# Optimization experiments

Measured on AMD Instinct MI355X. Metric: run time of the kernel, lower is better.

The kernel has to match this reference:

```python
import jax, jax.numpy as jnp
import numpy as np

ALPHA = 0.2      # GAT leaky_relu slope (args.alpha)
MLP_SLOPE = 0.01 # F.leaky_relu default in the MLP path
NEG = -9e15

def _l2_normalize(x, axis=1, eps=1e-12):
    n = jnp.sqrt(jnp.sum(x * x, axis=axis, keepdims=True))
    return x / jnp.maximum(n, eps)

def setup_inputs() -> dict:
    key = jax.random.key(0)
    ks = jax.random.split(key, 14)
    N, Din, Dh, H, Dg, M1, M2, E = 8192, 512, 256, 2, 512, 512, 256, 100000
    x = jax.random.normal(ks[0], (N, Din), dtype=jnp.float32)
    adj = jax.random.randint(ks[1], (N, N), 0, 2, dtype=jnp.int32)
    train_sample = jax.random.randint(ks[2], (E, 2), 0, N, dtype=jnp.int32)
    llm_emb = jax.random.normal(ks[3], (N, Dg), dtype=jnp.float32)
    # GAT head params (stacked over heads)
    Wg = jax.random.normal(ks[4], (H, Din, Dh), dtype=jnp.float32) * 0.05
    a1 = jax.random.normal(ks[5], (H, Dh), dtype=jnp.float32) * 0.05
    a2 = jax.random.normal(ks[6], (H, Dh), dtype=jnp.float32) * 0.05
    bias_g = jnp.zeros((H, Dh), dtype=jnp.float32)
    # MLP params
    W1 = jax.random.normal(ks[7], (Dh + Dg, M1), dtype=jnp.float32) * 0.03
    b1 = jnp.zeros((M1,), dtype=jnp.float32)
    W2 = jax.random.normal(ks[8], (M1, M2), dtype=jnp.float32) * 0.04
    b2 = jnp.zeros((M2,), dtype=jnp.float32)
    return {"x": x, "adj": adj, "train_sample": train_sample, "llm_emb": llm_emb,
            "Wg": Wg, "a1": a1, "a2": a2, "bias_g": bias_g,
            "W1": W1, "b1": b1, "W2": W2, "b2": b2}

def reference(x, adj, train_sample, llm_emb, Wg, a1, a2, bias_g, W1, b1, W2, b2):
    mask = adj > 0  # [N, N]

    def head(W, av1, av2, b):
        h = x @ W                                   # [N, Dh]
        s1 = h @ av1                                # [N]
        s2 = h @ av2                                # [N]
        e = jax.nn.leaky_relu(s1[:, None] + s2[None, :], ALPHA)  # [N, N]
        att = jax.nn.softmax(jnp.where(mask, e, NEG), axis=1)
        out = att @ h                               # [N, Dh]
        out = jax.nn.leaky_relu(out, ALPHA)
        out = _l2_normalize(out, axis=1)
        return out + b

    # encode: single GNN layer -> mean over heads (dropout inactive in eval)
    out_heads = jax.vmap(head)(Wg, a1, a2, bias_g)  # [H, N, Dh]
    embed_gnn = jnp.mean(out_heads, axis=0)         # [N, Dh]
    embed = jnp.concatenate([llm_emb, embed_gnn], axis=1)  # [N, Dg+Dh]

    def mlp(z):
        z = jax.nn.leaky_relu(z @ W1 + b1, MLP_SLOPE)
        z = jax.nn.leaky_relu(z @ W2 + b2, MLP_SLOPE)
        return z

    tf_embed = mlp(embed)
    target_embed = mlp(embed)
    train_tf = tf_embed[train_sample[:, 0]]
    train_tg = target_embed[train_sample[:, 1]]
    pred = jnp.sum(train_tf * train_tg, axis=1, keepdims=True)  # dot decode, [E,1]
    return pred
```

## Files before the change

kernel.cpp:

```cpp
#include <hip/hip_runtime.h>
#include <hip/hip_bf16.h>
#include <cstdint>
#include <cstddef>

#define ALPHA 0.2f
#define MLP_SLOPE 0.01f

typedef short bf16x8 __attribute__((ext_vector_type(8)));
typedef float f32x4 __attribute__((ext_vector_type(4)));
typedef unsigned short ushort_t;

#define ASM_BARRIER() __asm__ __volatile__("s_waitcnt lgkmcnt(0)\n\ts_barrier" ::: "memory")

__device__ __forceinline__ float lrelu(float x, float s) { return x > 0.f ? x : x * s; }
__device__ __forceinline__ ushort_t f2bf(float x) {
  __hip_bfloat16 h = __float2bfloat16(x);
  return *reinterpret_cast<ushort_t*>(&h);
}
__device__ __forceinline__ float bf2f(ushort_t u) {
  union { unsigned int i; float f; } v; v.i = ((unsigned int)u) << 16; return v.f;
}

__global__ __launch_bounds__(256) void tobf(
    const float* __restrict__ in, ushort_t* __restrict__ outp)
{
  int idx = blockIdx.x * 256 + threadIdx.x;
  float4 v = ((const float4*)in)[idx];
  ushort4 h;
  h.x = f2bf(v.x); h.y = f2bf(v.y); h.z = f2bf(v.z); h.w = f2bf(v.w);
  ((ushort4*)outp)[idx] = h;
}

__global__ __launch_bounds__(256) void zero_f(float* __restrict__ p)
{
  int idx = blockIdx.x * 256 + threadIdx.x;
  ((float4*)p)[idx] = make_float4(0.f, 0.f, 0.f, 0.f);
}

__global__ __launch_bounds__(256) void pack_wt(
    const float* __restrict__ W, ushort_t* __restrict__ hi,
    ushort_t* __restrict__ lo, int K, int N)
{
  int gid = blockIdx.x * 256 + threadIdx.x;
  int lane = gid & 63;
  int kbc = K >> 5;
  int kblk = (gid >> 6) % kbc;
  int nblk = (gid >> 6) / kbc;
  size_t b = (size_t)blockIdx.y * K * N;
  int col = nblk * 16 + (lane & 15);
  int krow = kblk * 32 + (lane >> 4) * 8;
  ushort_t h[8] __attribute__((aligned(16)));
  ushort_t l[8] __attribute__((aligned(16)));
#pragma unroll
  for (int e = 0; e < 8; ++e) {
    float v = W[b + (size_t)(krow + e) * N + col];
    h[e] = f2bf(v);
    l[e] = f2bf(v - bf2f(h[e]));
  }
  *(uint4*)&hi[b + (size_t)gid * 8] = *(uint4*)h;
  if (lo) *(uint4*)&lo[b + (size_t)gid * 8] = *(uint4*)l;
}

__global__ __launch_bounds__(256, 2) void gemm_h(
    const ushort_t* __restrict__ xb, const ushort_t* __restrict__ Wgp,
    const float* __restrict__ a1, const float* __restrict__ a2,
    ushort_t* __restrict__ Bpack, float* __restrict__ s1,
    float* __restrict__ s2)
{
  __shared__ ushort_t Ab[2][128][40];
  const int t = threadIdx.x;
  const int head = blockIdx.z;
  const int m0 = blockIdx.y * 128;
  const int n0 = blockIdx.x * 64;
  const int wave = t >> 6;
  const int wm = (wave & 1) * 64, wn = (wave >> 1) * 32;
  const int l16 = t & 15, quad = (t >> 4) & 3, l63 = t & 63;
  const int sr = t >> 1, sp = (t & 1) * 16;
  const ushort_t* arow_g = xb + (size_t)(m0 + sr) * 512 + sp;
  const ushort_t* bp = Wgp + (size_t)head * 256 * 512;
  const int nb0 = (n0 + wn) >> 4;

  f32x4 acc[4][2];
#pragma unroll
  for (int i = 0; i < 4; ++i)
#pragma unroll
    for (int j = 0; j < 2; ++j) acc[i][j] = (f32x4){0.f, 0.f, 0.f, 0.f};

  uint4 r0, r1;
  r0 = *(const uint4*)(arow_g);
  r1 = *(const uint4*)(arow_g + 8);
  *(uint4*)&Ab[0][sr][sp] = r0;
  *(uint4*)&Ab[0][sr][sp + 8] = r1;
  __syncthreads();

  for (int kb = 0; kb < 16; ++kb) {
    const int cur = kb & 1, nxt = cur ^ 1;
    if (kb < 15) {
      const ushort_t* p = arow_g + (kb + 1) * 32;
      r0 = *(const uint4*)p;
      r1 = *(const uint4*)(p + 8);
    }
    bf16x8 Bf[2];
#pragma unroll
    for (int nt = 0; nt < 2; ++nt)
      Bf[nt] = *(const bf16x8*)&bp[(((size_t)(nb0 + nt) * 16 + kb) * 64 + l63) * 8];
    bf16x8 Af[4];
#pragma unroll
    for (int mt = 0; mt < 4; ++mt)
      Af[mt] = *(const bf16x8*)&Ab[cur][wm + mt * 16 + l16][quad * 8];
#pragma unroll
    for (int mt = 0; mt < 4; ++mt)
#pragma unroll
      for (int nt = 0; nt < 2; ++nt)
        acc[mt][nt] = __builtin_amdgcn_mfma_f32_16x16x32_bf16(
            Af[mt], Bf[nt], acc[mt][nt], 0, 0, 0);
    if (kb < 15) {
      *(uint4*)&Ab[nxt][sr][sp] = r0;
      *(uint4*)&Ab[nxt][sr][sp + 8] = r1;
    }
    __syncthreads();
  }

#pragma unroll
  for (int mt = 0; mt < 4; ++mt)
#pragma unroll
    for (int nt = 0; nt < 2; ++nt)
#pragma unroll
      for (int rg = 0; rg < 4; ++rg) {
        int j = m0 + wm + mt * 16 + quad * 4 + rg;
        int c = n0 + wn + nt * 16 + l16;
        int kblk = j >> 5;
        int laneb = ((j >> 3) & 3) * 16 + (c & 15);
        int e = j & 7;
        Bpack[(((size_t)head * 256 + kblk) * 16 + (c >> 4)) * 512 + laneb * 8 + e] =
            f2bf(acc[mt][nt][rg]);
      }
  float a1v[2], a2v[2];
#pragma unroll
  for (int nt = 0; nt < 2; ++nt) {
    int c = n0 + wn + nt * 16 + l16;
    a1v[nt] = a1[head * 256 + c];
    a2v[nt] = a2[head * 256 + c];
  }
#pragma unroll
  for (int mt = 0; mt < 4; ++mt)
#pragma unroll
    for (int rg = 0; rg < 4; ++rg) {
      float p1 = acc[mt][0][rg] * a1v[0] + acc[mt][1][rg] * a1v[1];
      float p2 = acc[mt][0][rg] * a2v[0] + acc[mt][1][rg] * a2v[1];
      p1 += __shfl_xor(p1, 1); p2 += __shfl_xor(p2, 1);
      p1 += __shfl_xor(p1, 2); p2 += __shfl_xor(p2, 2);
      p1 += __shfl_xor(p1, 4); p2 += __shfl_xor(p2, 4);
      p1 += __shfl_xor(p1, 8); p2 += __shfl_xor(p2, 8);
      if (l16 == 0) {
        int row = m0 + wm + mt * 16 + quad * 4 + rg;
        atomicAdd(&s1[head * 8192 + row], p1);
        atomicAdd(&s2[head * 8192 + row], p2);
      }
    }
}

__global__ __launch_bounds__(256, 2) void gemm_mlp(
    const ushort_t* __restrict__ Ahi, const ushort_t* __restrict__ Alo,
    const ushort_t* __restrict__ Bph, const ushort_t* __restrict__ Bpl,
    const float* __restrict__ bias, float* __restrict__ Cf,
    ushort_t* __restrict__ Chi, ushort_t* __restrict__ Clo,
    int M, int N, int K, float slope)
{
  __shared__ ushort_t Ah[2][128][40], Al[2][128][40];
  const int kbc = K >> 5;
  const int t = threadIdx.x;
  const int m0 = blockIdx.y * 128;
  const int n0 = blockIdx.x * 64;
  const int wave = t >> 6;
  const int wm = (wave & 1) * 64, wn = (wave >> 1) * 32;
  const int l16 = t & 15, quad = (t >> 4) & 3, l63 = t & 63;
  const int sr = t >> 1, sp = (t & 1) * 16;
  const ushort_t* ah_g = Ahi + (size_t)(m0 + sr) * K + sp;
  const ushort_t* al_g = Alo + (size_t)(m0 + sr) * K + sp;
  const int nb0 = (n0 + wn) >> 4;

  f32x4 acc[4][2];
#pragma unroll
  for (int i = 0; i < 4; ++i)
#pragma unroll
    for (int j = 0; j < 2; ++j) acc[i][j] = (f32x4){0.f, 0.f, 0.f, 0.f};

  uint4 rh0, rh1, rl0, rl1;
  rh0 = *(const uint4*)(ah_g);
  rh1 = *(const uint4*)(ah_g + 8);
  rl0 = *(const uint4*)(al_g);
  rl1 = *(const uint4*)(al_g + 8);
  *(uint4*)&Ah[0][sr][sp] = rh0;
  *(uint4*)&Ah[0][sr][sp + 8] = rh1;
  *(uint4*)&Al[0][sr][sp] = rl0;
  *(uint4*)&Al[0][sr][sp + 8] = rl1;
  __syncthreads();

  for (int kb = 0; kb < kbc; ++kb) {
    const int cur = kb & 1, nxt = cur ^ 1;
    if (kb + 1 < kbc) {
      const ushort_t* ph = ah_g + (kb + 1) * 32;
      const ushort_t* plo = al_g + (kb + 1) * 32;
      rh0 = *(const uint4*)ph;
      rh1 = *(const uint4*)(ph + 8);
      rl0 = *(const uint4*)plo;
      rl1 = *(const uint4*)(plo + 8);
    }
    bf16x8 bh[2], bl[2];
#pragma unroll
    for (int nt = 0; nt < 2; ++nt) {
      size_t o = (((size_t)(nb0 + nt) * kbc + kb) * 64 + l63) * 8;
      bh[nt] = *(const bf16x8*)&Bph[o];
      bl[nt] = *(const bf16x8*)&Bpl[o];
    }
    bf16x8 afh[4], afl[4];
#pragma unroll
    for (int mt = 0; mt < 4; ++mt) {
      afh[mt] = *(const bf16x8*)&Ah[cur][wm + mt * 16 + l16][quad * 8];
      afl[mt] = *(const bf16x8*)&Al[cur][wm + mt * 16 + l16][quad * 8];
    }
#pragma unroll
    for (int mt = 0; mt < 4; ++mt)
#pragma unroll
      for (int nt = 0; nt < 2; ++nt) {
        acc[mt][nt] = __builtin_amdgcn_mfma_f32_16x16x32_bf16(afh[mt], bh[nt], acc[mt][nt], 0, 0, 0);
        acc[mt][nt] = __builtin_amdgcn_mfma_f32_16x16x32_bf16(afh[mt], bl[nt], acc[mt][nt], 0, 0, 0);
        acc[mt][nt] = __builtin_amdgcn_mfma_f32_16x16x32_bf16(afl[mt], bh[nt], acc[mt][nt], 0, 0, 0);
      }
    if (kb + 1 < kbc) {
      *(uint4*)&Ah[nxt][sr][sp] = rh0;
      *(uint4*)&Ah[nxt][sr][sp + 8] = rh1;
      *(uint4*)&Al[nxt][sr][sp] = rl0;
      *(uint4*)&Al[nxt][sr][sp + 8] = rl1;
    }
    __syncthreads();
  }

#pragma unroll
  for (int mt = 0; mt < 4; ++mt)
#pragma unroll
    for (int nt = 0; nt < 2; ++nt)
#pragma unroll
      for (int rg = 0; rg < 4; ++rg) {
        int m = m0 + wm + mt * 16 + quad * 4 + rg;
        int n = n0 + wn + nt * 16 + l16;
        float v = lrelu(acc[mt][nt][rg] + bias[n], slope);
        size_t o = (size_t)m * N + n;
        if (Cf) Cf[o] = v;
        if (Chi) {
          ushort_t h = f2bf(v);
          Chi[o] = h; Clo[o] = f2bf(v - bf2f(h));
        }
      }
}

__global__ __launch_bounds__(512, 4) void attn_mfma8(
    const ushort_t* __restrict__ Bpack, const float* __restrict__ s1g,
    const float* __restrict__ s2g, const int* __restrict__ adj,
    ushort_t* __restrict__ pacc, float* __restrict__ pl)
{
  __shared__ ushort_t Wlds[2][2][4][64][8];
  const int t = threadIdx.x;
  const int i0 = blockIdx.x * 64;
  const int js = blockIdx.y;
  const int kbase = js * 2048;
  const int ghead = t >> 8;
  const int wr = (t & 255) >> 2, kq = t & 3;
  const int glane = kq * 16 + (wr & 15);
  const int gmt = wr >> 4;
  const float s1v = s1g[ghead * 8192 + i0 + wr];
  const float* s2h = s2g + ghead * 8192;
  const int wave = t >> 6;
  const int chead = wave >> 2, nh = (wave >> 1) & 1, rg2 = wave & 1;
  const int l16 = t & 15, quad = (t >> 4) & 3;
  const int l63 = t & 63;
  f32x4 acc[2][8];
#pragma unroll
  for (int m = 0; m < 2; ++m)
#pragma unroll
    for (int n = 0; n < 8; ++n) acc[m][n] = (f32x4){0.f, 0.f, 0.f, 0.f};
  float rs = 0.f;

  const int* arow = adj + (size_t)(i0 + wr) * 8192;
  int4 pa0, pa1;
  float4 p2a, p2b;

  auto fetch = [&](int kk) {
    pa0 = *(const int4*)&arow[kk];
    pa1 = *(const int4*)&arow[kk + 4];
    p2a = *(const float4*)&s2h[kk];
    p2b = *(const float4*)&s2h[kk + 4];
  };
  auto gen = [&](int buf) {
    int am[8] = {pa0.x, pa0.y, pa0.z, pa0.w, pa1.x, pa1.y, pa1.z, pa1.w};
    float s2v[8] = {p2a.x, p2a.y, p2a.z, p2a.w, p2b.x, p2b.y, p2b.z, p2b.w};
    ushort_t w0[8] __attribute__((aligned(16)));
#pragma unroll
    for (int e = 0; e < 8; ++e) {
      float e0 = s1v + s2v[e];
      e0 = fmaxf(e0, 0.f) + ALPHA * fminf(e0, 0.f);
      float v0 = am[e] > 0 ? __expf(e0) : 0.f;
      rs += v0;
      w0[e] = f2bf(v0);
    }
    *(uint4*)&Wlds[buf][ghead][gmt][glane][0] = *(uint4*)w0;
  };
  auto mstep = [&](int buf, int kt) {
    const int kblk = js * 64 + kt;
    const ushort_t* bb =
        Bpack + ((((size_t)chead * 256 + kblk) * 16 + nh * 8) * 64 + l63) * 8;
    bf16x8 Af0 = *(const bf16x8*)&Wlds[buf][chead][rg2 * 2 + 0][l63][0];
    bf16x8 Af1 = *(const bf16x8*)&Wlds[buf][chead][rg2 * 2 + 1][l63][0];
    bf16x8 b0 = *(const bf16x8*)&bb[0];
#pragma unroll
    for (int nt = 0; nt < 8; ++nt) {
      bf16x8 bcur = b0;
      if (nt < 7) b0 = *(const bf16x8*)&bb[(nt + 1) * 512];
      acc[0][nt] = __builtin_amdgcn_mfma_f32_16x16x32_bf16(
          Af0, bcur, acc[0][nt], 0, 0, 0);
      acc[1][nt] = __builtin_amdgcn_mfma_f32_16x16x32_bf16(
          Af1, bcur, acc[1][nt], 0, 0, 0);
    }
  };

  fetch(kbase + kq * 8);
  gen(0);
  fetch(kbase + 32 + kq * 8);
  ASM_BARRIER();

  for (int kt = 0; kt < 64; ++kt) {
    const int cur = kt & 1, nxt = cur ^ 1;
    mstep(cur, kt);
    if (kt < 63) {
      gen(nxt);
      if (kt < 62) fetch(kbase + (kt + 2) * 32 + kq * 8);
    }
    ASM_BARRIER();
  }

  rs += __shfl_xor(rs, 1); rs += __shfl_xor(rs, 2);
  if (kq == 0)
    pl[((size_t)js * 2 + ghead) * 8192 + i0 + wr] = rs;
  const int n0 = nh * 128;
#pragma unroll
  for (int mt = 0; mt < 2; ++mt)
#pragma unroll
    for (int nt = 0; nt < 8; ++nt)
#pragma unroll
      for (int rg = 0; rg < 4; ++rg) {
        int row = i0 + rg2 * 32 + mt * 16 + quad * 4 + rg;
        int col = n0 + nt * 16 + l16;
        pacc[(((size_t)js * 2 + chead) * 8192 + row) * 256 + col] =
            f2bf(acc[mt][nt][rg]);
      }
}

__global__ __launch_bounds__(256) void attn_finalize(
    const ushort_t* __restrict__ pacc, const float* __restrict__ pl,
    const float* __restrict__ bg, const float* __restrict__ llm,
    ushort_t* __restrict__ ehi, ushort_t* __restrict__ elo)
{
  __shared__ float red[8];
  const int r = blockIdx.x;
  const int t = threadIdx.x;
  const int wv = t >> 6, lane = t & 63;
#pragma unroll
  for (int half = 0; half < 2; ++half) {
    float lv = llm[(size_t)r * 512 + half * 256 + t];
    ushort_t h = f2bf(lv);
    ehi[(size_t)r * 768 + half * 256 + t] = h;
    elo[(size_t)r * 768 + half * 256 + t] = f2bf(lv - bf2f(h));
  }
  float o[2];
#pragma unroll
  for (int hh = 0; hh < 2; ++hh) {
    float num = 0.f, l = 0.f;
#pragma unroll
    for (int js = 0; js < 4; ++js) {
      num += bf2f(pacc[(((size_t)js * 2 + hh) * 8192 + r) * 256 + t]);
      l += pl[((size_t)js * 2 + hh) * 8192 + r];
    }
    o[hh] = lrelu(num / l, ALPHA);
  }
  float v0 = o[0] * o[0], v1 = o[1] * o[1];
  for (int off = 32; off > 0; off >>= 1) {
    v0 += __shfl_xor(v0, off);
    v1 += __shfl_xor(v1, off);
  }
  if (lane == 0) { red[wv] = v0; red[4 + wv] = v1; }
  __syncthreads();
  float n0 = fmaxf(sqrtf(red[0] + red[1] + red[2] + red[3]), 1e-12f);
  float n1 = fmaxf(sqrtf(red[4] + red[5] + red[6] + red[7]), 1e-12f);
  float val = 0.5f * (o[0] / n0 + bg[t] + o[1] / n1 + bg[256 + t]);
  ushort_t h = f2bf(val);
  ehi[(size_t)r * 768 + 512 + t] = h;
  elo[(size_t)r * 768 + 512 + t] = f2bf(val - bf2f(h));
}

__global__ __launch_bounds__(256) void pred_kernel(
    const float* __restrict__ z2, const int* __restrict__ ts,
    float* __restrict__ out, int E)
{
  const int gw = (blockIdx.x * 256 + threadIdx.x) >> 6;
  const int lane = threadIdx.x & 63;
  if (gw >= E) return;
  const int a = ts[gw * 2], b = ts[gw * 2 + 1];
  float4 va = ((const float4*)(z2 + (size_t)a * 256))[lane];
  float4 vb = ((const float4*)(z2 + (size_t)b * 256))[lane];
  float p = va.x * vb.x + va.y * vb.y + va.z * vb.z + va.w * vb.w;
  for (int off = 32; off > 0; off >>= 1) p += __shfl_xor(p, off);
  if (lane == 0) out[gw] = p;
}

extern "C" void kernel_launch(void* const* d_in, const int* in_sizes, int n_in,
                              void* d_out, int out_size, void* d_ws, size_t ws_size,
                              hipStream_t stream) {
  const float* x   = (const float*)d_in[0];
  const int*   adj = (const int*)d_in[1];
  const int*   ts  = (const int*)d_in[2];
  const float* llm = (const float*)d_in[3];
  const float* Wg  = (const float*)d_in[4];
  const float* a1  = (const float*)d_in[5];
  const float* a2  = (const float*)d_in[6];
  const float* bg  = (const float*)d_in[7];
  const float* W1  = (const float*)d_in[8];
  const float* b1  = (const float*)d_in[9];
  const float* W2  = (const float*)d_in[10];
  const float* b2  = (const float*)d_in[11];
  float* out = (float*)d_out;
  float* ws  = (float*)d_ws;
  const int E = in_sizes[2] / 2;

  ushort_t* xb    = (ushort_t*)(ws + 0);
  ushort_t* Wgp   = (ushort_t*)(ws + 2097152);
  ushort_t* W1ph  = (ushort_t*)(ws + 2228224);
  ushort_t* W1pl  = (ushort_t*)(ws + 2424832);
  ushort_t* W2ph  = (ushort_t*)(ws + 2621440);
  ushort_t* W2pl  = (ushort_t*)(ws + 2686976);
  ushort_t* Bpack = (ushort_t*)(ws + 2752512);
  float*    s1    = ws + 4849664;
  float*    s2    = ws + 4866048;
  float*    pl    = ws + 4882432;
  ushort_t* pacc  = (ushort_t*)(ws + 4947968);
  ushort_t* ehi   = (ushort_t*)(ws + 13336576);
  ushort_t* elo   = (ushort_t*)(ws + 16482304);
  ushort_t* z1hi  = (ushort_t*)(ws + 19628032);
  ushort_t* z1lo  = (ushort_t*)(ws + 21725184);
  float*    z2    = ws + 23822336;

  tobf<<<4096, 256, 0, stream>>>(x, xb);
  pack_wt<<<dim3(64, 2), 256, 0, stream>>>(Wg, Wgp, nullptr, 512, 256);
  pack_wt<<<dim3(192, 1), 256, 0, stream>>>(W1, W1ph, W1pl, 768, 512);
  pack_wt<<<dim3(64, 1), 256, 0, stream>>>(W2, W2ph, W2pl, 512, 256);
  zero_f<<<32, 256, 0, stream>>>(s1);
  gemm_h<<<dim3(4, 64, 2), 256, 0, stream>>>(xb, Wgp, a1, a2, Bpack, s1, s2);
  attn_mfma8<<<dim3(128, 4), 512, 0, stream>>>(Bpack, s1, s2, adj, pacc, pl);
  attn_finalize<<<8192, 256, 0, stream>>>(pacc, pl, bg, llm, ehi, elo);
  gemm_mlp<<<dim3(8, 64), 256, 0, stream>>>(
      ehi, elo, W1ph, W1pl, b1, nullptr, z1hi, z1lo, 8192, 512, 768, MLP_SLOPE);
  gemm_mlp<<<dim3(4, 64), 256, 0, stream>>>(
      z1hi, z1lo, W2ph, W2pl, b2, z2, nullptr, nullptr, 8192, 256, 512, MLP_SLOPE);
  pred_kernel<<<(E * 64 + 255) / 256, 256, 0, stream>>>(z2, ts, out, E);
}
```

Before: 623.9 us.

## Generate attention A-fragments in registers and drop LDS staging in attention kernel

The attention kernel now has each wave compute its own bf16 attention-weight fragments directly in MFMA operand layout from adjacency and scores. This removes the LDS buffer and the per-iteration barrier, and uses register double-buffering of the global loads instead. Each block now covers 128 rows with the full 256 output columns per wave (16 accumulator tiles), so the grid halves and launch bounds drop to 1 block per SM. The cost is much higher register pressure and lower occupancy. Each head's adjacency and s2 data is also now read by both heads' waves separately rather than shared.

```diff
diff --git a/kernel.cpp b/kernel.cpp
--- a/kernel.cpp
+++ b/kernel.cpp
@@ -255,103 +255,110 @@
       }
 }
 
-__global__ __launch_bounds__(512, 4) void attn_mfma8(
+__global__ __launch_bounds__(512, 1) void attn_mfma8(
     const ushort_t* __restrict__ Bpack, const float* __restrict__ s1g,
     const float* __restrict__ s2g, const int* __restrict__ adj,
     ushort_t* __restrict__ pacc, float* __restrict__ pl)
 {
-  __shared__ ushort_t Wlds[2][2][4][64][8];
   const int t = threadIdx.x;
-  const int i0 = blockIdx.x * 64;
+  const int i0 = blockIdx.x * 128;
   const int js = blockIdx.y;
   const int kbase = js * 2048;
-  const int ghead = t >> 8;
-  const int wr = (t & 255) >> 2, kq = t & 3;
-  const int glane = kq * 16 + (wr & 15);
-  const int gmt = wr >> 4;
-  const float s1v = s1g[ghead * 8192 + i0 + wr];
-  const float* s2h = s2g + ghead * 8192;
   const int wave = t >> 6;
-  const int chead = wave >> 2, nh = (wave >> 1) & 1, rg2 = wave & 1;
-  const int l16 = t & 15, quad = (t >> 4) & 3;
+  const int head = wave >> 2;
+  const int rg8 = wave & 3;
   const int l63 = t & 63;
-  f32x4 acc[2][8];
+  const int l15 = t & 15;
+  const int oct = l63 >> 4;
+  const int row0 = i0 + rg8 * 32 + l15;
+  const float s1v0 = s1g[head * 8192 + row0];
+  const float s1v1 = s1g[head * 8192 + row0 + 16];
+  const float* s2h = s2g + head * 8192;
+  const int* arow0 = adj + (size_t)row0 * 8192;
+  const int* arow1 = arow0 + (size_t)16 * 8192;
+
+  f32x4 acc[2][16];
 #pragma unroll
   for (int m = 0; m < 2; ++m)
 #pragma unroll
-    for (int n = 0; n < 8; ++n) acc[m][n] = (f32x4){0.f, 0.f, 0.f, 0.f};
-  float rs = 0.f;
-
-  const int* arow = adj + (size_t)(i0 + wr) * 8192;
-  int4 pa0, pa1;
-  float4 p2a, p2b;
-
-  auto fetch = [&](int kk) {
-    pa0 = *(const int4*)&arow[kk];
-    pa1 = *(const int4*)&arow[kk + 4];
-    p2a = *(const float4*)&s2h[kk];
-    p2b = *(const float4*)&s2h[kk + 4];
+    for (int n = 0; n < 16; ++n) acc[m][n] = (f32x4){0.f, 0.f, 0.f, 0.f};
+  float rs0 = 0.f, rs1 = 0.f;
+
+  int4 A0a, A0b, A1a, A1b, B0a, B0b, B1a, B1b;
+  float4 Asa, Asb, Bsa, Bsb;
+
+  auto fetchA = [&](int kt) {
+    int c = kbase + kt * 32 + oct * 8;
+    A0a = *(const int4*)&arow0[c]; A0b = *(const int4*)&arow0[c + 4];
+    A1a = *(const int4*)&arow1[c]; A1b = *(const int4*)&arow1[c + 4];
+    Asa = *(const float4*)&s2h[c]; Asb = *(const float4*)&s2h[c + 4];
   };
-  auto gen = [&](int buf) {
-    int am[8] = {pa0.x, pa0.y, pa0.z, pa0.w, pa1.x, pa1.y, pa1.z, pa1.w};
-    float s2v[8] = {p2a.x, p2a.y, p2a.z, p2a.w, p2b.x, p2b.y, p2b.z, p2b.w};
-    ushort_t w0[8] __attribute__((aligned(16)));
+  auto fetchB = [&](int kt) {
+    int c = kbase + kt * 32 + oct * 8;
+    B0a = *(const int4*)&arow0[c]; B0b = *(const int4*)&arow0[c + 4];
+    B1a = *(const int4*)&arow1[c]; B1b = *(const int4*)&arow1[c + 4];
+    Bsa = *(const float4*)&s2h[c]; Bsb = *(const float4*)&s2h[c + 4];
+  };
+  auto genfrag = [&](int4 aa, int4 ab, float s1v, float4 sa, float4 sb,
+                     float& rs) -> bf16x8 {
+    int am[8] = {aa.x, aa.y, aa.z, aa.w, ab.x, ab.y, ab.z, ab.w};
+    float sv[8] = {sa.x, sa.y, sa.z, sa.w, sb.x, sb.y, sb.z, sb.w};
+    ushort_t w[8] __attribute__((aligned(16)));
 #pragma unroll
     for (int e = 0; e < 8; ++e) {
-      float e0 = s1v + s2v[e];
+      float e0 = s1v + sv[e];
       e0 = fmaxf(e0, 0.f) + ALPHA * fminf(e0, 0.f);
-      float v0 = am[e] > 0 ? __expf(e0) : 0.f;
-      rs += v0;
-      w0[e] = f2bf(v0);
-    }
-    *(uint4*)&Wlds[buf][ghead][gmt][glane][0] = *(uint4*)w0;
+      float v = am[e] > 0 ? __expf(e0) : 0.f;
+      rs += v;
+      w[e] = f2bf(v);
+    }
+    return *(bf16x8*)w;
   };
-  auto mstep = [&](int buf, int kt) {
-    const int kblk = js * 64 + kt;
+  auto mstep = [&](bf16x8 af0, bf16x8 af1, int kt) {
     const ushort_t* bb =
-        Bpack + ((((size_t)chead * 256 + kblk) * 16 + nh * 8) * 64 + l63) * 8;
-    bf16x8 Af0 = *(const bf16x8*)&Wlds[buf][chead][rg2 * 2 + 0][l63][0];
-    bf16x8 Af1 = *(const bf16x8*)&Wlds[buf][chead][rg2 * 2 + 1][l63][0];
-    bf16x8 b0 = *(const bf16x8*)&bb[0];
-#pragma unroll
-    for (int nt = 0; nt < 8; ++nt) {
-      bf16x8 bcur = b0;
-      if (nt < 7) b0 = *(const bf16x8*)&bb[(nt + 1) * 512];
+        Bpack + (((size_t)head * 256 + (js * 64 + kt)) * 16 * 64 + l63) * 8;
+    bf16x8 Bq[4];
+#pragma unroll
+    for (int q = 0; q < 4; ++q) Bq[q] = *(const bf16x8*)&bb[q * 512];
+#pragma unroll
+    for (int nt = 0; nt < 16; ++nt) {
+      bf16x8 bcur = Bq[nt & 3];
+      if (nt < 12) Bq[nt & 3] = *(const bf16x8*)&bb[(nt + 4) * 512];
       acc[0][nt] = __builtin_amdgcn_mfma_f32_16x16x32_bf16(
-          Af0, bcur, acc[0][nt], 0, 0, 0);
+          af0, bcur, acc[0][nt], 0, 0, 0);
       acc[1][nt] = __builtin_amdgcn_mfma_f32_16x16x32_bf16(
-          Af1, bcur, acc[1][nt], 0, 0, 0);
+          af1, bcur, acc[1][nt], 0, 0, 0);
     }
   };
 
-  fetch(kbase + kq * 8);
-  gen(0);
-  fetch(kbase + 32 + kq * 8);
-  ASM_BARRIER();
-
-  for (int kt = 0; kt < 64; ++kt) {
-    const int cur = kt & 1, nxt = cur ^ 1;
-    mstep(cur, kt);
-    if (kt < 63) {
-      gen(nxt);
-      if (kt < 62) fetch(kbase + (kt + 2) * 32 + kq * 8);
-    }
-    ASM_BARRIER();
-  }
-
-  rs += __shfl_xor(rs, 1); rs += __shfl_xor(rs, 2);
-  if (kq == 0)
-    pl[((size_t)js * 2 + ghead) * 8192 + i0 + wr] = rs;
-  const int n0 = nh * 128;
+  fetchA(0);
+#pragma unroll 1
+  for (int kt = 0; kt < 64; kt += 2) {
+    fetchB(kt + 1);
+    bf16x8 a0 = genfrag(A0a, A0b, s1v0, Asa, Asb, rs0);
+    bf16x8 a1 = genfrag(A1a, A1b, s1v1, Asa, Asb, rs1);
+    mstep(a0, a1, kt);
+    if (kt + 2 < 64) fetchA(kt + 2);
+    bf16x8 b0 = genfrag(B0a, B0b, s1v0, Bsa, Bsb, rs0);
+    bf16x8 b1 = genfrag(B1a, B1b, s1v1, Bsa, Bsb, rs1);
+    mstep(b0, b1, kt + 1);
+  }
+
+  rs0 += __shfl_xor(rs0, 16); rs0 += __shfl_xor(rs0, 32);
+  rs1 += __shfl_xor(rs1, 16); rs1 += __shfl_xor(rs1, 32);
+  if (oct == 0) {
+    pl[((size_t)js * 2 + head) * 8192 + row0] = rs0;
+    pl[((size_t)js * 2 + head) * 8192 + row0 + 16] = rs1;
+  }
 #pragma unroll
   for (int mt = 0; mt < 2; ++mt)
 #pragma unroll
-    for (int nt = 0; nt < 8; ++nt)
+    for (int nt = 0; nt < 16; ++nt)
 #pragma unroll
       for (int rg = 0; rg < 4; ++rg) {
-        int row = i0 + rg2 * 32 + mt * 16 + quad * 4 + rg;
-        int col = n0 + nt * 16 + l16;
-        pacc[(((size_t)js * 2 + chead) * 8192 + row) * 256 + col] =
+        int row = i0 + rg8 * 32 + mt * 16 + oct * 4 + rg;
+        int col = nt * 16 + l15;
+        pacc[(((size_t)js * 2 + head) * 8192 + row) * 256 + col] =
             f2bf(acc[mt][nt][rg]);
       }
 }
@@ -455,7 +462,7 @@
   pack_wt<<<dim3(64, 1), 256, 0, stream>>>(W2, W2ph, W2pl, 512, 256);
   zero_f<<<32, 256, 0, stream>>>(s1);
   gemm_h<<<dim3(4, 64, 2), 256, 0, stream>>>(xb, Wgp, a1, a2, Bpack, s1, s2);
-  attn_mfma8<<<dim3(128, 4), 512, 0, stream>>>(Bpack, s1, s2, adj, pacc, pl);
+  attn_mfma8<<<dim3(64, 4), 512, 0, stream>>>(Bpack, s1, s2, adj, pacc, pl);
   attn_finalize<<<8192, 256, 0, stream>>>(pacc, pl, bg, llm, ehi, elo);
   gemm_mlp<<<dim3(8, 64), 256, 0, stream>>>(
       ehi, elo, W1ph, W1pl, b1, nullptr, z1hi, z1lo, 8192, 512, 768, MLP_SLOPE);
```

Measured after the change: 659.7 us. 5.7% more time.
